# Optimization experiments

Hardware: AMD Instinct MI355X
Metric: run time of the kernel (lower is better)

## Reference

```python
import jax, jax.numpy as jnp
import numpy as np

N_NODES = 50000


def _sage_conv(x, src, dst, Wl, bl, Wr):
    # mean aggregation of neighbor (source) features at destination nodes
    msg = x[src]                                              # [E, d]
    agg = jax.ops.segment_sum(msg, dst, num_segments=N_NODES)  # [N, d]
    cnt = jax.ops.segment_sum(jnp.ones((src.shape[0],), x.dtype), dst,
                              num_segments=N_NODES)            # [N]
    agg = agg / jnp.clip(cnt, 1.0)[:, None]
    # lin_l(aggregated) + lin_r(self), bias only on lin_l (PyG default)
    return agg @ Wl + bl + x @ Wr


def setup_inputs() -> dict:
    key = jax.random.key(0)
    ks = jax.random.split(key, 8)
    d = 128
    E = 800000
    x = jax.random.normal(ks[0], (N_NODES, d), dtype=jnp.float32)
    edge_index = jax.random.randint(ks[1], (2, E), 0, N_NODES, dtype=jnp.int64)
    s1 = 1.0 / np.sqrt(d)
    s2 = 1.0 / np.sqrt(32)
    return {
        "x": x,
        "edge_index": edge_index,
        "W1l": jax.random.normal(ks[2], (d, 32), jnp.float32) * s1,
        "b1": jnp.zeros((32,), jnp.float32),
        "W1r": jax.random.normal(ks[3], (d, 32), jnp.float32) * s1,
        "W2l": jax.random.normal(ks[4], (32, 32), jnp.float32) * s2,
        "b2": jnp.zeros((32,), jnp.float32),
        "W2r": jax.random.normal(ks[5], (32, 32), jnp.float32) * s2,
    }


def reference(x, edge_index, W1l, b1, W1r, W2l, b2, W2r):
    src, dst = edge_index[0], edge_index[1]
    h = jax.nn.relu(_sage_conv(x, src, dst, W1l, b1, W1r))
    return _sage_conv(h, src, dst, W2l, b2, W2r)
```

## Files before the change

kernel.cpp:

```cpp
#include <hip/hip_runtime.h>
#include <hip/hip_bf16.h>


#define N_NODES 50000
#define NB 196
#define GB 256

__global__ __launch_bounds__(256) void kproj(
    const float* __restrict__ in, const float* __restrict__ Wl,
    const float* __restrict__ Wr, float* __restrict__ z, int N, int K) {
  __shared__ float xs[64 * 68];
  __shared__ float ws[64 * 64];
  const int t = threadIdx.x;
  const int n0 = blockIdx.x * 64;
  const int nvalid = (N - n0) < 64 ? (N - n0) : 64;

  const int tx = t & 15, ty = t >> 4;
  const int c0 = tx * 4;
  const int nl = ty * 4;

  float acc[4][4];
#pragma unroll
  for (int i = 0; i < 4; i++)
#pragma unroll
    for (int j = 0; j < 4; j++) acc[i][j] = 0.f;

  for (int kc = 0; kc < K; kc += 64) {
    const int KC = (K - kc) < 64 ? (K - kc) : 64;
    for (int i = t; i < KC * 32; i += 256) {
      int k = i >> 5, c = i & 31;
      ws[k * 64 + c] = Wl[(size_t)(kc + k) * 32 + c];
      ws[k * 64 + 32 + c] = Wr[(size_t)(kc + k) * 32 + c];
    }
    {
      const int kq = KC >> 2;
      const int sh = (KC == 64) ? 4 : 3;
      const int lim = nvalid * kq;
      for (int i = t; i < lim; i += 256) {
        int n = i >> sh, q = i & (kq - 1);
        float4 v = *(const float4*)(in + (size_t)(n0 + n) * K + kc + q * 4);
        *(float4*)(xs + n * 68 + q * 4) = v;
      }
    }
    __syncthreads();

    const float* x0 = xs + (nl + 0) * 68;
    const float* x1 = xs + (nl + 1) * 68;
    const float* x2 = xs + (nl + 2) * 68;
    const float* x3 = xs + (nl + 3) * 68;
    for (int k = 0; k < KC; k += 4) {
      float4 xa = *(const float4*)(x0 + k);
      float4 xb = *(const float4*)(x1 + k);
      float4 xc = *(const float4*)(x2 + k);
      float4 xd = *(const float4*)(x3 + k);
#pragma unroll
      for (int kk = 0; kk < 4; kk++) {
        float4 w = *(const float4*)(ws + (k + kk) * 64 + c0);
        float va = ((const float*)&xa)[kk];
        float vb = ((const float*)&xb)[kk];
        float vc = ((const float*)&xc)[kk];
        float vd = ((const float*)&xd)[kk];
        acc[0][0] += va * w.x; acc[0][1] += va * w.y;
        acc[0][2] += va * w.z; acc[0][3] += va * w.w;
        acc[1][0] += vb * w.x; acc[1][1] += vb * w.y;
        acc[1][2] += vb * w.z; acc[1][3] += vb * w.w;
        acc[2][0] += vc * w.x; acc[2][1] += vc * w.y;
        acc[2][2] += vc * w.z; acc[2][3] += vc * w.w;
        acc[3][0] += vd * w.x; acc[3][1] += vd * w.y;
        acc[3][2] += vd * w.z; acc[3][3] += vd * w.w;
      }
    }
    __syncthreads();
  }
#pragma unroll
  for (int i = 0; i < 4; i++) {
    int node = n0 + nl + i;
    if (node < N) {
      float4 v = make_float4(acc[i][0], acc[i][1], acc[i][2], acc[i][3]);
      *(float4*)(z + (size_t)node * 64 + c0) = v;
    }
  }
}

__global__ __launch_bounds__(256) void k_bcount(const int* __restrict__ dst,
                                                int* __restrict__ blkhist,
                                                int E, int chunk) {
  __shared__ int h[NB];
  const int t = threadIdx.x, b = blockIdx.x;
  if (t < NB) h[t] = 0;
  __syncthreads();
  const int e0 = b * chunk;
  int e1 = e0 + chunk;
  if (e1 > E) e1 = E;
  for (int e = e0 + t; e < e1; e += 256) atomicAdd(&h[dst[e] >> 8], 1);
  __syncthreads();
  if (t < NB) blkhist[b * NB + t] = h[t];
}

__global__ __launch_bounds__(256) void k_bscan(int* __restrict__ blkhist,
                                               int* __restrict__ bb, int E) {
  __shared__ int sc[256];
  const int t = threadIdx.x;
  int run = 0;
  if (t < NB) {
    for (int b = 0; b < GB; b += 8) {
      int v[8];
#pragma unroll
      for (int i = 0; i < 8; i++) v[i] = blkhist[(b + i) * NB + t];
#pragma unroll
      for (int i = 0; i < 8; i++) {
        blkhist[(b + i) * NB + t] = run;
        run += v[i];
      }
    }
  }
  sc[t] = (t < NB) ? run : 0;
  __syncthreads();
  for (int off = 1; off < 256; off <<= 1) {
    int tmp = (t >= off) ? sc[t - off] : 0;
    __syncthreads();
    sc[t] += tmp;
    __syncthreads();
  }
  if (t < NB) bb[t] = sc[t] - run;
  if (t == 0) bb[NB] = E;
}

__global__ __launch_bounds__(256) void k_bscatter(
    const int* __restrict__ src, const int* __restrict__ dst,
    const int* __restrict__ blkhist, const int* __restrict__ bb,
    int* __restrict__ ebuf, int E, int chunk) {
  __shared__ int cur[NB];
  const int t = threadIdx.x, b = blockIdx.x;
  if (t < NB) cur[t] = bb[t] + blkhist[b * NB + t];
  __syncthreads();
  const int e0 = b * chunk;
  int e1 = e0 + chunk;
  if (e1 > E) e1 = E;
  for (int e = e0 + t; e < e1; e += 256) {
    int d = dst[e], s = src[e];
    int pos = atomicAdd(&cur[d >> 8], 1);
    ebuf[pos] = (s << 8) | (d & 255);
  }
}

__global__ __launch_bounds__(256) void k_bsort(const int* __restrict__ ebuf,
                                               const int* __restrict__ bb,
                                               int* __restrict__ adj,
                                               int* __restrict__ row_ptr,
                                               int N, int E) {
  __shared__ int cnt[256];
  __shared__ int sc[256];
  const int t = threadIdx.x, k = blockIdx.x;
  const int r0 = bb[k], r1 = bb[k + 1];
  cnt[t] = 0;
  __syncthreads();
  for (int i = r0 + t; i < r1; i += 256) atomicAdd(&cnt[ebuf[i] & 255], 1);
  __syncthreads();
  sc[t] = cnt[t];
  __syncthreads();
  for (int off = 1; off < 256; off <<= 1) {
    int tmp = (t >= off) ? sc[t - off] : 0;
    __syncthreads();
    sc[t] += tmp;
    __syncthreads();
  }
  const int excl = sc[t] - cnt[t];
  const int node = (k << 8) + t;
  if (node < N) row_ptr[node] = r0 + excl;
  if (k == 0 && t == 0) row_ptr[N] = E;
  __syncthreads();
  cnt[t] = r0 + excl;
  __syncthreads();
  for (int i = r0 + t; i < r1; i += 256) {
    int v = ebuf[i];
    int pos = atomicAdd(&cnt[v & 255], 1);
    adj[pos] = v >> 8;
  }
}

__global__ __launch_bounds__(256) void k_agg(
    const float* __restrict__ zc, const int* __restrict__ adj,
    const int* __restrict__ row_ptr, const float* __restrict__ bias,
    float* __restrict__ out, int N, int do_relu) {
  const int t = threadIdx.x;
  const int j = t & 31;
  const int node = blockIdx.x * 8 + (t >> 5);
  if (node >= N) return;
  const int r0 = row_ptr[node], r1 = row_ptr[node + 1];
  float a0 = 0.f, a1 = 0.f, a2 = 0.f, a3 = 0.f;
  int e = r0;
  for (; e + 4 <= r1; e += 4) {
    int s0 = adj[e], s1 = adj[e + 1], s2 = adj[e + 2], s3 = adj[e + 3];
    a0 += zc[(size_t)s0 * 64 + j];
    a1 += zc[(size_t)s1 * 64 + j];
    a2 += zc[(size_t)s2 * 64 + j];
    a3 += zc[(size_t)s3 * 64 + j];
  }
  for (; e < r1; ++e) a0 += zc[(size_t)adj[e] * 64 + j];
  float sum = (a0 + a1) + (a2 + a3);
  const int deg = r1 - r0;
  float m = sum / (float)(deg > 1 ? deg : 1);
  float v = m + bias[j] + zc[(size_t)node * 64 + 32 + j];
  out[(size_t)node * 32 + j] = do_relu ? fmaxf(v, 0.f) : v;
}

extern "C" void kernel_launch(void* const* d_in, const int* in_sizes, int n_in,
                              void* d_out, int out_size, void* d_ws,
                              size_t ws_size, hipStream_t stream) {
  const float* x = (const float*)d_in[0];
  const int* ei = (const int*)d_in[1];
  const float* W1l = (const float*)d_in[2];
  const float* b1 = (const float*)d_in[3];
  const float* W1r = (const float*)d_in[4];
  const float* W2l = (const float*)d_in[5];
  const float* b2 = (const float*)d_in[6];
  const float* W2r = (const float*)d_in[7];
  float* out = (float*)d_out;

  const int N = N_NODES;
  const int E = in_sizes[1] / 2;

  float* zc = (float*)d_ws;
  int* ebuf = (int*)(zc + (size_t)N * 64);
  int* adj = ebuf + E;
  int* row_ptr = adj + E;
  int* bb = row_ptr + N + 1;
  int* blkhist = bb + NB + 1;
  float* h = out;

  const int* srcp = ei;
  const int* dstp = ei + E;

  const int chunk = (E + GB - 1) / GB;
  const int nblk_proj = (N + 63) / 64;
  const int nblk_agg = (N + 7) / 8;

  k_bcount<<<GB, 256, 0, stream>>>(dstp, blkhist, E, chunk);
  k_bscan<<<1, 256, 0, stream>>>(blkhist, bb, E);
  k_bscatter<<<GB, 256, 0, stream>>>(srcp, dstp, blkhist, bb, ebuf, E, chunk);
  k_bsort<<<NB, 256, 0, stream>>>(ebuf, bb, adj, row_ptr, N, E);

  kproj<<<nblk_proj, 256, 0, stream>>>(x, W1l, W1r, zc, N, 128);
  k_agg<<<nblk_agg, 256, 0, stream>>>(zc, adj, row_ptr, b1, h, N, 1);
  kproj<<<nblk_proj, 256, 0, stream>>>(h, W2l, W2r, zc, N, 32);
  k_agg<<<nblk_agg, 256, 0, stream>>>(zc, adj, row_ptr, b2, out, N, 0);
}
```

Baseline: 188.1 us.

## Store gathered projections in bf16 and fuse layer-1 aggregation with layer-2 projection

The projected neighbor features are now stored as bf16 in a separate 32-wide array, which halves the bytes moved by the random gathers in both aggregation passes. The self term stays in fp32 in its own array. The layer-1 aggregation is fused with the layer-2 projection in one kernel that keeps h in shared memory, removing a launch and a round trip of h through global memory. The block histogram is also transposed so the scan reads contiguous int4 vectors. Rounding the messages to bf16 adds precision error, and the fused kernel processes 64 nodes per block with one warp per 8 nodes, which may reduce latency hiding in the gather.

```diff
diff --git a/kernel.cpp b/kernel.cpp
--- a/kernel.cpp
+++ b/kernel.cpp
@@ -6,18 +6,25 @@
 #define NB 196
 #define GB 256
 
+__device__ __forceinline__ unsigned short f2bf(float f) {
+  unsigned int u = __float_as_uint(f);
+  return (unsigned short)((u + 0x7fffu + ((u >> 16) & 1u)) >> 16);
+}
+__device__ __forceinline__ float bf2f(unsigned short v) {
+  return __uint_as_float(((unsigned int)v) << 16);
+}
+
 __global__ __launch_bounds__(256) void kproj(
     const float* __restrict__ in, const float* __restrict__ Wl,
-    const float* __restrict__ Wr, float* __restrict__ z, int N, int K) {
+    const float* __restrict__ Wr, unsigned short* __restrict__ zn,
+    float* __restrict__ zs, int N, int K) {
   __shared__ float xs[64 * 68];
   __shared__ float ws[64 * 64];
   const int t = threadIdx.x;
   const int n0 = blockIdx.x * 64;
   const int nvalid = (N - n0) < 64 ? (N - n0) : 64;
-
   const int tx = t & 15, ty = t >> 4;
-  const int c0 = tx * 4;
-  const int nl = ty * 4;
+  const int c0 = tx * 4, nl = ty * 4;
 
   float acc[4][4];
 #pragma unroll
@@ -43,7 +50,6 @@
       }
     }
     __syncthreads();
-
     const float* x0 = xs + (nl + 0) * 68;
     const float* x1 = xs + (nl + 1) * 68;
     const float* x2 = xs + (nl + 2) * 68;
@@ -76,8 +82,15 @@
   for (int i = 0; i < 4; i++) {
     int node = n0 + nl + i;
     if (node < N) {
-      float4 v = make_float4(acc[i][0], acc[i][1], acc[i][2], acc[i][3]);
-      *(float4*)(z + (size_t)node * 64 + c0) = v;
+      if (tx < 8) {
+        ushort4 p;
+        p.x = f2bf(acc[i][0]); p.y = f2bf(acc[i][1]);
+        p.z = f2bf(acc[i][2]); p.w = f2bf(acc[i][3]);
+        *(ushort4*)(zn + (size_t)node * 32 + c0) = p;
+      } else {
+        *(float4*)(zs + (size_t)node * 32 + (c0 - 32)) =
+            make_float4(acc[i][0], acc[i][1], acc[i][2], acc[i][3]);
+      }
     }
   }
 }
@@ -94,7 +107,7 @@
   if (e1 > E) e1 = E;
   for (int e = e0 + t; e < e1; e += 256) atomicAdd(&h[dst[e] >> 8], 1);
   __syncthreads();
-  if (t < NB) blkhist[b * NB + t] = h[t];
+  if (t < NB) blkhist[t * GB + b] = h[t];
 }
 
 __global__ __launch_bounds__(256) void k_bscan(int* __restrict__ blkhist,
@@ -103,15 +116,15 @@
   const int t = threadIdx.x;
   int run = 0;
   if (t < NB) {
-    for (int b = 0; b < GB; b += 8) {
-      int v[8];
-#pragma unroll
-      for (int i = 0; i < 8; i++) v[i] = blkhist[(b + i) * NB + t];
-#pragma unroll
-      for (int i = 0; i < 8; i++) {
-        blkhist[(b + i) * NB + t] = run;
-        run += v[i];
-      }
+    int4* p = (int4*)(blkhist + t * GB);
+    for (int q = 0; q < GB / 4; q++) {
+      int4 v = p[q];
+      int4 o;
+      o.x = run; run += v.x;
+      o.y = run; run += v.y;
+      o.z = run; run += v.z;
+      o.w = run; run += v.w;
+      p[q] = o;
     }
   }
   sc[t] = (t < NB) ? run : 0;
@@ -132,7 +145,7 @@
     int* __restrict__ ebuf, int E, int chunk) {
   __shared__ int cur[NB];
   const int t = threadIdx.x, b = blockIdx.x;
-  if (t < NB) cur[t] = bb[t] + blkhist[b * NB + t];
+  if (t < NB) cur[t] = bb[t] + blkhist[t * GB + b];
   __syncthreads();
   const int e0 = b * chunk;
   int e1 = e0 + chunk;
@@ -179,10 +192,100 @@
   }
 }
 
-__global__ __launch_bounds__(256) void k_agg(
-    const float* __restrict__ zc, const int* __restrict__ adj,
-    const int* __restrict__ row_ptr, const float* __restrict__ bias,
-    float* __restrict__ out, int N, int do_relu) {
+__global__ __launch_bounds__(256) void k_aggproj(
+    const unsigned short* __restrict__ zn1, const float* __restrict__ zs1,
+    const int* __restrict__ adj, const int* __restrict__ row_ptr,
+    const float* __restrict__ b1, const float* __restrict__ W2l,
+    const float* __restrict__ W2r, unsigned short* __restrict__ zn2,
+    float* __restrict__ zs2, int N) {
+  __shared__ float hs[64 * 36];
+  __shared__ float ws2[32 * 64];
+  const int t = threadIdx.x;
+  const int n0 = blockIdx.x * 64;
+  for (int i = t; i < 32 * 32; i += 256) {
+    int k = i >> 5, c = i & 31;
+    ws2[k * 64 + c] = W2l[k * 32 + c];
+    ws2[k * 64 + 32 + c] = W2r[k * 32 + c];
+  }
+  const int j = t & 31, hw = t >> 5;
+  const float bj = b1[j];
+  for (int p = 0; p < 8; p++) {
+    int node = n0 + hw * 8 + p;
+    float v = 0.f;
+    if (node < N) {
+      int r0 = row_ptr[node], r1 = row_ptr[node + 1];
+      float a0 = 0.f, a1 = 0.f, a2 = 0.f, a3 = 0.f;
+      int e = r0;
+      for (; e + 4 <= r1; e += 4) {
+        int s0 = adj[e], s1 = adj[e + 1], s2 = adj[e + 2], s3 = adj[e + 3];
+        a0 += bf2f(zn1[(size_t)s0 * 32 + j]);
+        a1 += bf2f(zn1[(size_t)s1 * 32 + j]);
+        a2 += bf2f(zn1[(size_t)s2 * 32 + j]);
+        a3 += bf2f(zn1[(size_t)s3 * 32 + j]);
+      }
+      for (; e < r1; ++e) a0 += bf2f(zn1[(size_t)adj[e] * 32 + j]);
+      float sum = (a0 + a1) + (a2 + a3);
+      int deg = r1 - r0;
+      v = sum / (float)(deg > 1 ? deg : 1) + bj + zs1[(size_t)node * 32 + j];
+      v = fmaxf(v, 0.f);
+    }
+    hs[(hw * 8 + p) * 36 + j] = v;
+  }
+  __syncthreads();
+  const int tx = t & 15, ty = t >> 4;
+  const int c0 = tx * 4, nl = ty * 4;
+  float acc[4][4];
+#pragma unroll
+  for (int i = 0; i < 4; i++)
+#pragma unroll
+    for (int jj = 0; jj < 4; jj++) acc[i][jj] = 0.f;
+  const float* x0 = hs + (nl + 0) * 36;
+  const float* x1 = hs + (nl + 1) * 36;
+  const float* x2 = hs + (nl + 2) * 36;
+  const float* x3 = hs + (nl + 3) * 36;
+  for (int k = 0; k < 32; k += 4) {
+    float4 xa = *(const float4*)(x0 + k);
+    float4 xb = *(const float4*)(x1 + k);
+    float4 xc = *(const float4*)(x2 + k);
+    float4 xd = *(const float4*)(x3 + k);
+#pragma unroll
+    for (int kk = 0; kk < 4; kk++) {
+      float4 w = *(const float4*)(ws2 + (k + kk) * 64 + c0);
+      float va = ((const float*)&xa)[kk];
+      float vb = ((const float*)&xb)[kk];
+      float vc = ((const float*)&xc)[kk];
+      float vd = ((const float*)&xd)[kk];
+      acc[0][0] += va * w.x; acc[0][1] += va * w.y;
+      acc[0][2] += va * w.z; acc[0][3] += va * w.w;
+      acc[1][0] += vb * w.x; acc[1][1] += vb * w.y;
+      acc[1][2] += vb * w.z; acc[1][3] += vb * w.w;
+      acc[2][0] += vc * w.x; acc[2][1] += vc * w.y;
+      acc[2][2] += vc * w.z; acc[2][3] += vc * w.w;
+      acc[3][0] += vd * w.x; acc[3][1] += vd * w.y;
+      acc[3][2] += vd * w.z; acc[3][3] += vd * w.w;
+    }
+  }
+#pragma unroll
+  for (int i = 0; i < 4; i++) {
+    int node = n0 + nl + i;
+    if (node < N) {
+      if (tx < 8) {
+        ushort4 p;
+        p.x = f2bf(acc[i][0]); p.y = f2bf(acc[i][1]);
+        p.z = f2bf(acc[i][2]); p.w = f2bf(acc[i][3]);
+        *(ushort4*)(zn2 + (size_t)node * 32 + c0) = p;
+      } else {
+        *(float4*)(zs2 + (size_t)node * 32 + (c0 - 32)) =
+            make_float4(acc[i][0], acc[i][1], acc[i][2], acc[i][3]);
+      }
+    }
+  }
+}
+
+__global__ __launch_bounds__(256) void k_agg2(
+    const unsigned short* __restrict__ zn, const float* __restrict__ zs,
+    const int* __restrict__ adj, const int* __restrict__ row_ptr,
+    const float* __restrict__ bias, float* __restrict__ out, int N) {
   const int t = threadIdx.x;
   const int j = t & 31;
   const int node = blockIdx.x * 8 + (t >> 5);
@@ -192,17 +295,16 @@
   int e = r0;
   for (; e + 4 <= r1; e += 4) {
     int s0 = adj[e], s1 = adj[e + 1], s2 = adj[e + 2], s3 = adj[e + 3];
-    a0 += zc[(size_t)s0 * 64 + j];
-    a1 += zc[(size_t)s1 * 64 + j];
-    a2 += zc[(size_t)s2 * 64 + j];
-    a3 += zc[(size_t)s3 * 64 + j];
-  }
-  for (; e < r1; ++e) a0 += zc[(size_t)adj[e] * 64 + j];
+    a0 += bf2f(zn[(size_t)s0 * 32 + j]);
+    a1 += bf2f(zn[(size_t)s1 * 32 + j]);
+    a2 += bf2f(zn[(size_t)s2 * 32 + j]);
+    a3 += bf2f(zn[(size_t)s3 * 32 + j]);
+  }
+  for (; e < r1; ++e) a0 += bf2f(zn[(size_t)adj[e] * 32 + j]);
   float sum = (a0 + a1) + (a2 + a3);
   const int deg = r1 - r0;
   float m = sum / (float)(deg > 1 ? deg : 1);
-  float v = m + bias[j] + zc[(size_t)node * 64 + 32 + j];
-  out[(size_t)node * 32 + j] = do_relu ? fmaxf(v, 0.f) : v;
+  out[(size_t)node * 32 + j] = m + bias[j] + zs[(size_t)node * 32 + j];
 }
 
 extern "C" void kernel_launch(void* const* d_in, const int* in_sizes, int n_in,
@@ -221,13 +323,15 @@
   const int N = N_NODES;
   const int E = in_sizes[1] / 2;
 
-  float* zc = (float*)d_ws;
-  int* ebuf = (int*)(zc + (size_t)N * 64);
+  float* zs1 = (float*)d_ws;
+  float* zs2 = zs1 + (size_t)N * 32;
+  unsigned short* zn1 = (unsigned short*)(zs2 + (size_t)N * 32);
+  unsigned short* zn2 = zn1 + (size_t)N * 32;
+  int* ebuf = (int*)(zn2 + (size_t)N * 32);
   int* adj = ebuf + E;
   int* row_ptr = adj + E;
   int* bb = row_ptr + N + 1;
-  int* blkhist = bb + NB + 1;
-  float* h = out;
+  int* blkhist = (int*)(((size_t)(bb + NB + 1) + 15) & ~(size_t)15);
 
   const int* srcp = ei;
   const int* dstp = ei + E;
@@ -241,8 +345,8 @@
   k_bscatter<<<GB, 256, 0, stream>>>(srcp, dstp, blkhist, bb, ebuf, E, chunk);
   k_bsort<<<NB, 256, 0, stream>>>(ebuf, bb, adj, row_ptr, N, E);
 
-  kproj<<<nblk_proj, 256, 0, stream>>>(x, W1l, W1r, zc, N, 128);
-  k_agg<<<nblk_agg, 256, 0, stream>>>(zc, adj, row_ptr, b1, h, N, 1);
-  kproj<<<nblk_proj, 256, 0, stream>>>(h, W2l, W2r, zc, N, 32);
-  k_agg<<<nblk_agg, 256, 0, stream>>>(zc, adj, row_ptr, b2, out, N, 0);
-}
+  kproj<<<nblk_proj, 256, 0, stream>>>(x, W1l, W1r, zn1, zs1, N, 128);
+  k_aggproj<<<nblk_proj, 256, 0, stream>>>(zn1, zs1, adj, row_ptr, b1, W2l,
+                                           W2r, zn2, zs2, N);
+  k_agg2<<<nblk_agg, 256, 0, stream>>>(zn2, zs2, adj, row_ptr, b2, out, N);
+}
```

New measurement: 230.8 us. 1.23x slower.

## Store neighbor projections in bf16 split layout and transpose block histogram

Applied to the files above, without the earlier changes.

The projection kernel now writes the aggregated-side half (lin_l output) as bf16 into a compact 32-wide array and the self half as fp32 into a separate array. Each gather row per edge drops from a 256-byte stride to a 64-byte contiguous bf16 row, and the aggregation loop is unrolled to 8 edges. The block histogram is also transposed so the single-block scan reads contiguous int4 vectors. Rounding neighbor features to bf16 before the mean adds precision loss to both layers.

```diff
diff --git a/kernel.cpp b/kernel.cpp
--- a/kernel.cpp
+++ b/kernel.cpp
@@ -6,18 +6,25 @@
 #define NB 196
 #define GB 256
 
+__device__ __forceinline__ unsigned short f2bf(float f) {
+  unsigned int u = __float_as_uint(f);
+  return (unsigned short)((u + 0x7fffu + ((u >> 16) & 1u)) >> 16);
+}
+__device__ __forceinline__ float bf2f(unsigned short v) {
+  return __uint_as_float(((unsigned int)v) << 16);
+}
+
 __global__ __launch_bounds__(256) void kproj(
     const float* __restrict__ in, const float* __restrict__ Wl,
-    const float* __restrict__ Wr, float* __restrict__ z, int N, int K) {
+    const float* __restrict__ Wr, unsigned short* __restrict__ zn,
+    float* __restrict__ zs, int N, int K) {
   __shared__ float xs[64 * 68];
   __shared__ float ws[64 * 64];
   const int t = threadIdx.x;
   const int n0 = blockIdx.x * 64;
   const int nvalid = (N - n0) < 64 ? (N - n0) : 64;
-
   const int tx = t & 15, ty = t >> 4;
-  const int c0 = tx * 4;
-  const int nl = ty * 4;
+  const int c0 = tx * 4, nl = ty * 4;
 
   float acc[4][4];
 #pragma unroll
@@ -43,7 +50,6 @@
       }
     }
     __syncthreads();
-
     const float* x0 = xs + (nl + 0) * 68;
     const float* x1 = xs + (nl + 1) * 68;
     const float* x2 = xs + (nl + 2) * 68;
@@ -76,8 +82,15 @@
   for (int i = 0; i < 4; i++) {
     int node = n0 + nl + i;
     if (node < N) {
-      float4 v = make_float4(acc[i][0], acc[i][1], acc[i][2], acc[i][3]);
-      *(float4*)(z + (size_t)node * 64 + c0) = v;
+      if (tx < 8) {
+        ushort4 p;
+        p.x = f2bf(acc[i][0]); p.y = f2bf(acc[i][1]);
+        p.z = f2bf(acc[i][2]); p.w = f2bf(acc[i][3]);
+        *(ushort4*)(zn + (size_t)node * 32 + c0) = p;
+      } else {
+        *(float4*)(zs + (size_t)node * 32 + (c0 - 32)) =
+            make_float4(acc[i][0], acc[i][1], acc[i][2], acc[i][3]);
+      }
     }
   }
 }
@@ -94,7 +107,7 @@
   if (e1 > E) e1 = E;
   for (int e = e0 + t; e < e1; e += 256) atomicAdd(&h[dst[e] >> 8], 1);
   __syncthreads();
-  if (t < NB) blkhist[b * NB + t] = h[t];
+  if (t < NB) blkhist[t * GB + b] = h[t];
 }
 
 __global__ __launch_bounds__(256) void k_bscan(int* __restrict__ blkhist,
@@ -103,15 +116,15 @@
   const int t = threadIdx.x;
   int run = 0;
   if (t < NB) {
-    for (int b = 0; b < GB; b += 8) {
-      int v[8];
-#pragma unroll
-      for (int i = 0; i < 8; i++) v[i] = blkhist[(b + i) * NB + t];
-#pragma unroll
-      for (int i = 0; i < 8; i++) {
-        blkhist[(b + i) * NB + t] = run;
-        run += v[i];
-      }
+    int4* p = (int4*)(blkhist + t * GB);
+    for (int q = 0; q < GB / 4; q++) {
+      int4 v = p[q];
+      int4 o;
+      o.x = run; run += v.x;
+      o.y = run; run += v.y;
+      o.z = run; run += v.z;
+      o.w = run; run += v.w;
+      p[q] = o;
     }
   }
   sc[t] = (t < NB) ? run : 0;
@@ -132,7 +145,7 @@
     int* __restrict__ ebuf, int E, int chunk) {
   __shared__ int cur[NB];
   const int t = threadIdx.x, b = blockIdx.x;
-  if (t < NB) cur[t] = bb[t] + blkhist[b * NB + t];
+  if (t < NB) cur[t] = bb[t] + blkhist[t * GB + b];
   __syncthreads();
   const int e0 = b * chunk;
   int e1 = e0 + chunk;
@@ -180,9 +193,10 @@
 }
 
 __global__ __launch_bounds__(256) void k_agg(
-    const float* __restrict__ zc, const int* __restrict__ adj,
-    const int* __restrict__ row_ptr, const float* __restrict__ bias,
-    float* __restrict__ out, int N, int do_relu) {
+    const unsigned short* __restrict__ zn, const float* __restrict__ zs,
+    const int* __restrict__ adj, const int* __restrict__ row_ptr,
+    const float* __restrict__ bias, float* __restrict__ out, int N,
+    int do_relu) {
   const int t = threadIdx.x;
   const int j = t & 31;
   const int node = blockIdx.x * 8 + (t >> 5);
@@ -190,19 +204,29 @@
   const int r0 = row_ptr[node], r1 = row_ptr[node + 1];
   float a0 = 0.f, a1 = 0.f, a2 = 0.f, a3 = 0.f;
   int e = r0;
-  for (; e + 4 <= r1; e += 4) {
-    int s0 = adj[e], s1 = adj[e + 1], s2 = adj[e + 2], s3 = adj[e + 3];
-    a0 += zc[(size_t)s0 * 64 + j];
-    a1 += zc[(size_t)s1 * 64 + j];
-    a2 += zc[(size_t)s2 * 64 + j];
-    a3 += zc[(size_t)s3 * 64 + j];
-  }
-  for (; e < r1; ++e) a0 += zc[(size_t)adj[e] * 64 + j];
+  for (; e + 8 <= r1; e += 8) {
+    int s0 = adj[e + 0], s1 = adj[e + 1], s2 = adj[e + 2], s3 = adj[e + 3];
+    int s4 = adj[e + 4], s5 = adj[e + 5], s6 = adj[e + 6], s7 = adj[e + 7];
+    float g0 = bf2f(zn[(size_t)s0 * 32 + j]);
+    float g1 = bf2f(zn[(size_t)s1 * 32 + j]);
+    float g2 = bf2f(zn[(size_t)s2 * 32 + j]);
+    float g3 = bf2f(zn[(size_t)s3 * 32 + j]);
+    float g4 = bf2f(zn[(size_t)s4 * 32 + j]);
+    float g5 = bf2f(zn[(size_t)s5 * 32 + j]);
+    float g6 = bf2f(zn[(size_t)s6 * 32 + j]);
+    float g7 = bf2f(zn[(size_t)s7 * 32 + j]);
+    a0 += g0 + g4;
+    a1 += g1 + g5;
+    a2 += g2 + g6;
+    a3 += g3 + g7;
+  }
+  for (; e < r1; ++e) a0 += bf2f(zn[(size_t)adj[e] * 32 + j]);
   float sum = (a0 + a1) + (a2 + a3);
   const int deg = r1 - r0;
-  float m = sum / (float)(deg > 1 ? deg : 1);
-  float v = m + bias[j] + zc[(size_t)node * 64 + 32 + j];
-  out[(size_t)node * 32 + j] = do_relu ? fmaxf(v, 0.f) : v;
+  float v = sum / (float)(deg > 1 ? deg : 1) + bias[j] +
+            zs[(size_t)node * 32 + j];
+  if (do_relu) v = fmaxf(v, 0.f);
+  out[(size_t)node * 32 + j] = v;
 }
 
 extern "C" void kernel_launch(void* const* d_in, const int* in_sizes, int n_in,
@@ -221,13 +245,15 @@
   const int N = N_NODES;
   const int E = in_sizes[1] / 2;
 
-  float* zc = (float*)d_ws;
-  int* ebuf = (int*)(zc + (size_t)N * 64);
+  float* zs1 = (float*)d_ws;
+  float* zs2 = zs1 + (size_t)N * 32;
+  unsigned short* zn1 = (unsigned short*)(zs2 + (size_t)N * 32);
+  unsigned short* zn2 = zn1 + (size_t)N * 32;
+  int* ebuf = (int*)(zn2 + (size_t)N * 32);
   int* adj = ebuf + E;
   int* row_ptr = adj + E;
   int* bb = row_ptr + N + 1;
-  int* blkhist = bb + NB + 1;
-  float* h = out;
+  int* blkhist = (int*)(((size_t)(bb + NB + 1) + 15) & ~(size_t)15);
 
   const int* srcp = ei;
   const int* dstp = ei + E;
@@ -241,8 +267,8 @@
   k_bscatter<<<GB, 256, 0, stream>>>(srcp, dstp, blkhist, bb, ebuf, E, chunk);
   k_bsort<<<NB, 256, 0, stream>>>(ebuf, bb, adj, row_ptr, N, E);
 
-  kproj<<<nblk_proj, 256, 0, stream>>>(x, W1l, W1r, zc, N, 128);
-  k_agg<<<nblk_agg, 256, 0, stream>>>(zc, adj, row_ptr, b1, h, N, 1);
-  kproj<<<nblk_proj, 256, 0, stream>>>(h, W2l, W2r, zc, N, 32);
-  k_agg<<<nblk_agg, 256, 0, stream>>>(zc, adj, row_ptr, b2, out, N, 0);
-}
+  kproj<<<nblk_proj, 256, 0, stream>>>(x, W1l, W1r, zn1, zs1, N, 128);
+  k_agg<<<nblk_agg, 256, 0, stream>>>(zn1, zs1, adj, row_ptr, b1, out, N, 1);
+  kproj<<<nblk_proj, 256, 0, stream>>>(out, W2l, W2r, zn2, zs2, N, 32);
+  k_agg<<<nblk_agg, 256, 0, stream>>>(zn2, zs2, adj, row_ptr, b2, out, N, 0);
+}
```

New measurement: 192.2 us. +2.2%, slower.
